# Optimization experiments

Hardware: AMD Instinct MI355X
Metric: run time of the kernel (lower is better)

Reference implementation:

```python
import jax, jax.numpy as jnp
import numpy as np

B, N, M = 16, 2048, 2048


def setup_inputs() -> dict:
    key = jax.random.key(0)
    k1, k2, k3 = jax.random.split(key, 3)
    pred_dsmat = jax.random.uniform(k1, (B, N, M), dtype=jnp.float32)
    # valid sizes: src_ns <= tgt_ns so a permutation GT exists for every valid row
    src_ns = jax.random.randint(k2, (B,), 1024, 1537, dtype=jnp.int32)
    tgt_ns = jax.random.randint(k3, (B,), 1537, 2049, dtype=jnp.int32)
    # gt_perm: identity permutation restricted to the valid region (one 1 per valid row)
    i = jnp.arange(N)[:, None]
    j = jnp.arange(M)[None, :]
    eye = (i == j).astype(jnp.float32)  # [N, M]
    row_mask = (jnp.arange(N)[None, :] < src_ns[:, None]).astype(jnp.float32)  # [B, N]
    gt_perm = eye[None, :, :] * row_mask[:, :, None]  # [B, N, M]
    return {"pred_dsmat": pred_dsmat, "gt_perm": gt_perm,
            "src_ns": src_ns, "tgt_ns": tgt_ns, "beta_value": 0.1}


def reference(pred_dsmat, gt_perm, src_ns, tgt_ns, beta_value):
    Bn, Nn, Mn = pred_dsmat.shape
    row_mask = jnp.arange(Nn)[None, :] < src_ns[:, None]   # [B, N] bool
    col_mask = jnp.arange(Mn)[None, :] < tgt_ns[:, None]   # [B, M] bool
    mask = row_mask[:, :, None] & col_mask[:, None, :]     # [B, N, M]

    pred = jnp.clip(pred_dsmat, 0.0, 1.0) * mask
    gt = gt_perm * mask

    gt_pred = pred * gt                      # gt-selected predicted values
    row_gt = gt_pred.sum(axis=2)             # [B, N] per-row GT value
    col_gt = gt_pred.sum(axis=1)             # [B, M] per-col GT value
    row_cnt = gt.sum(axis=2)                 # [B, N] #GT matches per row
    col_cnt = gt.sum(axis=1)                 # [B, M] #GT matches per col

    # attention masks: entries >= (gt value - beta), restricted to valid region
    att_src = ((pred >= row_gt[:, :, None] - beta_value) & mask) * row_cnt[:, :, None]
    att_tgt = ((pred >= col_gt[:, None, :] - beta_value) & mask) * col_cnt[:, None, :]

    src_neg = jnp.sum(((att_src - gt) * pred) ** 2, axis=2)  # [B, N]
    src_pos = jnp.sum(gt_pred ** 2, axis=2)                  # [B, N]
    tgt_neg = jnp.sum(((att_tgt - gt) * pred) ** 2, axis=1)  # [B, M]

    # sum of tgt_neg over the GT-matched column of each row == dot with column counts
    corr = jnp.einsum('bm,bm->b', tgt_neg, col_cnt)          # [B]

    denom = 1.0 + src_neg + corr[:, None]                    # [B, N]
    num = jnp.where(row_mask, src_pos, 1.0)
    den = jnp.where(row_mask, denom, 1.0)
    loss = -0.5 * jnp.sum(jnp.log(num / den) * row_mask)
    n_sum = src_ns.sum().astype(pred.dtype)
    return loss / n_sum
```

## Files before the change

### kernel.cpp

```cpp
#include <hip/hip_runtime.h>

#define B_ 16
#define N_ 2048
#define M_ 2048
#define ROWS 32
#define WROWS 8
#define KCAP 4

__device__ __forceinline__ float wave_sum(float v) {
#pragma unroll
    for (int off = 32; off >= 1; off >>= 1) v += __shfl_xor(v, off);
    return v;
}

extern "C" __global__ __launch_bounds__(256) void k_gt(
    const float* __restrict__ gt,
    const int* __restrict__ src_ns, const int* __restrict__ tgt_ns,
    int* __restrict__ nnz, int* __restrict__ ent_col,
    float* __restrict__ ent_val, int* flag)
{
    const int b = blockIdx.y;
    const int src = src_ns[b];
    const int band = blockIdx.x;
    if (band * ROWS >= src) return;
    const int tgt = tgt_ns[b];
    const int wave = threadIdx.x >> 6, lane = threadIdx.x & 63;
    const int base = b * (N_ * M_);
    const int jmax = (tgt + 255) >> 8;

    const int row0 = band * ROWS + wave * WROWS;
    for (int r = 0; r < WROWS; ++r) {
        const int n = row0 + r;
        if (n >= src) break;
        const int ri = b * N_ + n;
        const float4* grow = (const float4*)(gt + base + n * M_);
        for (int j = 0; j < jmax; ++j) {
            const int m4 = j * 64 + lane;
            const float4 g4 = grow[m4];
            if (g4.x != 0.f || g4.y != 0.f || g4.z != 0.f || g4.w != 0.f) {
                const int mb = m4 * 4;
#define GC(KK, MB) do { \
    const int c = mb + KK; \
    const float gv = g4.MB; \
    if (gv != 0.f && c < tgt) { \
        const int slot = atomicAdd(&nnz[ri], 1); \
        if (slot < KCAP) { ent_col[ri * KCAP + slot] = c; ent_val[ri * KCAP + slot] = gv; } \
        else *flag = 1; \
    } \
} while (0)
                GC(0, x); GC(1, y); GC(2, z); GC(3, w);
#undef GC
            }
        }
    }
}

extern "C" __global__ __launch_bounds__(256) void k_mid(
    const float* __restrict__ pred,
    const int* __restrict__ src_ns,
    const int* __restrict__ nnz, const int* __restrict__ ent_col,
    const float* __restrict__ ent_val, const int* flag,
    float* __restrict__ row_gt, float* __restrict__ row_cnt,
    float* __restrict__ col_gt, float* __restrict__ col_cnt)
{
    if (*flag) return;
    const int ri = blockIdx.x * 256 + threadIdx.x;
    const int b = ri >> 11, n = ri & (N_ - 1);
    if (n >= src_ns[b]) { row_gt[ri] = 0.f; row_cnt[ri] = 0.f; return; }
    const int nn0 = nnz[ri];
    const int nn = nn0 < KCAP ? nn0 : KCAP;
    float rg = 0.f, rc = 0.f;
    for (int s = 0; s < nn; ++s) {
        const int c = ent_col[ri * KCAP + s];
        const float gv = ent_val[ri * KCAP + s];
        float p = pred[b * (N_ * M_) + n * M_ + c];
        p = fminf(fmaxf(p, 0.f), 1.f);
        rg += gv * p; rc += gv;
        atomicAdd(&col_gt[b * M_ + c], gv * p);
        atomicAdd(&col_cnt[b * M_ + c], gv);
    }
    row_gt[ri] = rg; row_cnt[ri] = rc;
}

extern "C" __global__ __launch_bounds__(256) void k_p1d(
    const float* __restrict__ pred, const float* __restrict__ gt,
    const int* __restrict__ src_ns, const int* __restrict__ tgt_ns,
    const int* flag,
    float* __restrict__ row_gt, float* __restrict__ row_cnt,
    float* __restrict__ col_gt, float* __restrict__ col_cnt)
{
    if (*flag == 0) return;
    const int b = blockIdx.y;
    const int src = src_ns[b];
    const int band = blockIdx.x;
    if (band * ROWS >= src) return;
    const int tgt = tgt_ns[b];
    const int wave = threadIdx.x >> 6, lane = threadIdx.x & 63;
    const int base = b * (N_ * M_);

    float4 acg[8], accn[8];
#pragma unroll
    for (int j = 0; j < 8; ++j) { acg[j] = make_float4(0,0,0,0); accn[j] = make_float4(0,0,0,0); }

    const int row0 = band * ROWS + wave * WROWS;
    for (int r = 0; r < WROWS; ++r) {
        const int n = row0 + r;
        if (n >= src) break;
        const float4* prow = (const float4*)(pred + base + n * M_);
        const float4* grow = (const float4*)(gt + base + n * M_);
        float rg = 0.f, rc = 0.f;
#pragma unroll
        for (int j = 0; j < 8; ++j) {
            const int m4 = j * 64 + lane;
            const float4 p4 = prow[m4];
            const float4 g4 = grow[m4];
            const int mb = m4 * 4;
#define P1C(KK, MB) do { \
    const bool ok = (mb + KK) < tgt; \
    float p = fminf(fmaxf(p4.MB, 0.f), 1.f); p = ok ? p : 0.f; \
    const float g = ok ? g4.MB : 0.f; \
    const float gp = p * g; \
    rg += gp; rc += g; \
    acg[j].MB += gp; accn[j].MB += g; \
} while (0)
            P1C(0, x); P1C(1, y); P1C(2, z); P1C(3, w);
#undef P1C
        }
        rg = wave_sum(rg); rc = wave_sum(rc);
        if (lane == 0) { row_gt[b * N_ + n] = rg; row_cnt[b * N_ + n] = rc; }
    }

    __shared__ float4 s_cg[M_ / 4];
    __shared__ float4 s_cc[M_ / 4];
    for (int i = threadIdx.x; i < M_ / 4; i += 256) {
        s_cg[i] = make_float4(0,0,0,0);
        s_cc[i] = make_float4(0,0,0,0);
    }
    __syncthreads();
    for (int w = 0; w < 4; ++w) {
        if (wave == w) {
#pragma unroll
            for (int j = 0; j < 8; ++j) {
                const int i = j * 64 + lane;
                float4 v = s_cg[i];
                v.x += acg[j].x; v.y += acg[j].y; v.z += acg[j].z; v.w += acg[j].w;
                s_cg[i] = v;
                float4 u = s_cc[i];
                u.x += accn[j].x; u.y += accn[j].y; u.z += accn[j].z; u.w += accn[j].w;
                s_cc[i] = u;
            }
        }
        __syncthreads();
    }
    const float* fcg = (const float*)s_cg;
    const float* fcc = (const float*)s_cc;
    for (int i = threadIdx.x; i < M_; i += 256) {
        atomicAdd(&col_gt[b * M_ + i], fcg[i]);
        atomicAdd(&col_cnt[b * M_ + i], fcc[i]);
    }
}

extern "C" __global__ __launch_bounds__(256) void k_pred(
    const float* __restrict__ pred, const float* __restrict__ gt,
    const int* __restrict__ src_ns, const int* __restrict__ tgt_ns,
    const float* __restrict__ beta_p,
    const float* __restrict__ row_gt, const float* __restrict__ row_cnt,
    const float* __restrict__ col_gt, const float* __restrict__ col_cnt,
    const int* __restrict__ nnz, const int* __restrict__ ent_col,
    const float* __restrict__ ent_val, const int* flag,
    float* __restrict__ src_neg, float* __restrict__ src_pos,
    float* __restrict__ tgt_neg)
{
    const int b = blockIdx.y;
    const int src = src_ns[b];
    const int band = blockIdx.x;
    if (band * ROWS >= src) return;
    const int tgt = tgt_ns[b];
    const float beta = beta_p[0];
    const int wave = threadIdx.x >> 6, lane = threadIdx.x & 63;
    const int base = b * (N_ * M_);
    const bool dense = (*flag != 0);
    const int jmax = (tgt + 255) >> 8;

    float4 cgb[8], cc[8], tn[8];
    const float4* cg4 = (const float4*)(col_gt + b * M_);
    const float4* cc4 = (const float4*)(col_cnt + b * M_);
#pragma unroll
    for (int j = 0; j < 8; ++j) {
        float4 v = cg4[j * 64 + lane];
        v.x -= beta; v.y -= beta; v.z -= beta; v.w -= beta;
        cgb[j] = v;
        cc[j] = cc4[j * 64 + lane];
        tn[j] = make_float4(0,0,0,0);
    }

    const int row0 = band * ROWS + wave * WROWS;
    if (!dense) {
        for (int r = 0; r < WROWS; ++r) {
            const int n = row0 + r;
            if (n >= src) break;
            const int ri = b * N_ + n;
            const float rc = row_cnt[ri];
            const float rth = row_gt[ri] - beta;
            const float4* prow = (const float4*)(pred + base + n * M_);
            float sneg = 0.f, spos = 0.f;
#pragma unroll
            for (int j = 0; j < 8; ++j) {
                if (j < jmax) {
                    const int m4 = j * 64 + lane;
                    const float4 p4 = prow[m4];
                    const int mb = m4 * 4;
#define P2S(KK, MB) do { \
    const bool ok = (mb + KK) < tgt; \
    float p = fminf(fmaxf(p4.MB, 0.f), 1.f); p = ok ? p : 0.f; \
    const float as = (p >= rth) ? rc : 0.f; \
    const float ds = as * p; \
    sneg += ds * ds; \
    const float at = (p >= cgb[j].MB) ? cc[j].MB : 0.f; \
    const float d = at * p; \
    tn[j].MB += d * d; \
} while (0)
                    P2S(0, x); P2S(1, y); P2S(2, z); P2S(3, w);
#undef P2S
                }
            }
            sneg = wave_sum(sneg);
            if (lane == 0) {
                const int nn0 = nnz[ri];
                const int nn = nn0 < KCAP ? nn0 : KCAP;
                for (int s = 0; s < nn; ++s) {
                    const int c = ent_col[ri * KCAP + s];
                    const float gv = ent_val[ri * KCAP + s];
                    float pv = pred[base + n * M_ + c];
                    pv = fminf(fmaxf(pv, 0.f), 1.f);
                    const float as = (pv >= rth) ? rc : 0.f;
                    const float d0 = as * pv;
                    const float d1 = (as - gv) * pv;
                    sneg += d1 * d1 - d0 * d0;
                    const float gp = gv * pv;
                    spos += gp * gp;
                    const float at = (pv >= col_gt[b * M_ + c] - beta) ? col_cnt[b * M_ + c] : 0.f;
                    const float t0 = at * pv;
                    const float t1 = (at - gv) * pv;
                    atomicAdd(&tgt_neg[b * M_ + c], t1 * t1 - t0 * t0);
                }
                src_neg[ri] = sneg; src_pos[ri] = spos;
            }
        }
    } else {
        for (int r = 0; r < WROWS; ++r) {
            const int n = row0 + r;
            if (n >= src) break;
            const int ri = b * N_ + n;
            const float rc = row_cnt[ri];
            const float rth = row_gt[ri] - beta;
            const float4* prow = (const float4*)(pred + base + n * M_);
            const float4* grow = (const float4*)(gt + base + n * M_);
            float sneg = 0.f, spos = 0.f;
#pragma unroll
            for (int j = 0; j < 8; ++j) {
                const int m4 = j * 64 + lane;
                const float4 p4 = prow[m4];
                const float4 g4 = grow[m4];
                const int mb = m4 * 4;
#define P2D(KK, MB) do { \
    const bool ok = (mb + KK) < tgt; \
    float p = fminf(fmaxf(p4.MB, 0.f), 1.f); p = ok ? p : 0.f; \
    const float gv = ok ? g4.MB : 0.f; \
    const float as = (p >= rth) ? rc : 0.f; \
    const float ds = (as - gv) * p; \
    sneg += ds * ds; \
    const float gp = gv * p; spos += gp * gp; \
    const float at = (p >= cgb[j].MB) ? cc[j].MB : 0.f; \
    const float dt = (at - gv) * p; \
    tn[j].MB += dt * dt; \
} while (0)
                P2D(0, x); P2D(1, y); P2D(2, z); P2D(3, w);
#undef P2D
            }
            sneg = wave_sum(sneg); spos = wave_sum(spos);
            if (lane == 0) { src_neg[ri] = sneg; src_pos[ri] = spos; }
        }
    }

    __shared__ float4 s_tn[M_ / 4];
    for (int i = threadIdx.x; i < M_ / 4; i += 256) s_tn[i] = make_float4(0,0,0,0);
    __syncthreads();
    for (int w = 0; w < 4; ++w) {
        if (wave == w) {
#pragma unroll
            for (int j = 0; j < 8; ++j) {
                const int i = j * 64 + lane;
                float4 v = s_tn[i];
                v.x += tn[j].x; v.y += tn[j].y; v.z += tn[j].z; v.w += tn[j].w;
                s_tn[i] = v;
            }
        }
        __syncthreads();
    }
    const float* ftn = (const float*)s_tn;
    for (int i = threadIdx.x; i < M_; i += 256)
        atomicAdd(&tgt_neg[b * M_ + i], ftn[i]);
}

extern "C" __global__ __launch_bounds__(256) void k_final(
    const float* __restrict__ src_neg, const float* __restrict__ src_pos,
    const float* __restrict__ tgt_neg, const float* __restrict__ col_cnt,
    const int* __restrict__ src_ns, float* __restrict__ out)
{
    const int b = blockIdx.x;
    const int wave = threadIdx.x >> 6, lane = threadIdx.x & 63;
    __shared__ float sredc[4];
    __shared__ float sredl[4];

    float c = 0.f;
    for (int i = threadIdx.x; i < M_; i += 256)
        c += tgt_neg[b * M_ + i] * col_cnt[b * M_ + i];
    c = wave_sum(c);
    if (lane == 0) sredc[wave] = c;
    __syncthreads();
    const float corr = sredc[0] + sredc[1] + sredc[2] + sredc[3];

    const int src = src_ns[b];
    float ls = 0.f;
    for (int n = threadIdx.x; n < src; n += 256) {
        const float sp = src_pos[b * N_ + n];
        const float sn = src_neg[b * N_ + n];
        ls += logf(sp) - logf(1.f + sn + corr);
    }
    ls = wave_sum(ls);
    if (lane == 0) sredl[wave] = ls;
    __syncthreads();
    if (threadIdx.x == 0) {
        const float total = sredl[0] + sredl[1] + sredl[2] + sredl[3];
        float nsum = 0.f;
        for (int i = 0; i < B_; ++i) nsum += (float)src_ns[i];
        atomicAdd(out, -0.5f * total / nsum);
    }
}

extern "C" void kernel_launch(void* const* d_in, const int* in_sizes, int n_in,
                              void* d_out, int out_size, void* d_ws, size_t ws_size,
                              hipStream_t stream)
{
    const float* pred   = (const float*)d_in[0];
    const float* gtp    = (const float*)d_in[1];
    const int*   src_ns = (const int*)d_in[2];
    const int*   tgt_ns = (const int*)d_in[3];
    const float* beta   = (const float*)d_in[4];
    float* out = (float*)d_out;
    float* ws  = (float*)d_ws;

    float* col_gt  = ws;
    float* col_cnt = col_gt  + B_ * M_;
    float* tgt_neg = col_cnt + B_ * M_;
    int*   nnz     = (int*)(tgt_neg + B_ * M_);
    int*   flag    = nnz + B_ * N_;
    float* row_gt  = (float*)(flag + 1);
    float* row_cnt = row_gt  + B_ * N_;
    float* src_neg = row_cnt + B_ * N_;
    float* src_pos = src_neg + B_ * N_;
    int*   ent_col = (int*)(src_pos + B_ * N_);
    float* ent_val = (float*)(ent_col + B_ * N_ * KCAP);

    const size_t zero_bytes = (size_t)(3 * B_ * M_ + B_ * N_ + 1) * sizeof(float);
    hipMemsetAsync(d_ws, 0, zero_bytes, stream);
    hipMemsetAsync(d_out, 0, sizeof(float), stream);

    dim3 grid(N_ / ROWS, B_);
    k_gt<<<grid, 256, 0, stream>>>(gtp, src_ns, tgt_ns, nnz, ent_col, ent_val, flag);
    k_mid<<<(B_ * N_) / 256, 256, 0, stream>>>(pred, src_ns, nnz, ent_col, ent_val, flag,
                                               row_gt, row_cnt, col_gt, col_cnt);
    k_p1d<<<grid, 256, 0, stream>>>(pred, gtp, src_ns, tgt_ns, flag,
                                    row_gt, row_cnt, col_gt, col_cnt);
    k_pred<<<grid, 256, 0, stream>>>(pred, gtp, src_ns, tgt_ns, beta,
                                     row_gt, row_cnt, col_gt, col_cnt,
                                     nnz, ent_col, ent_val, flag,
                                     src_neg, src_pos, tgt_neg);
    k_final<<<B_, 256, 0, stream>>>(src_neg, src_pos, tgt_neg, col_cnt, src_ns, out);
}
```

Before: 581.2 us.

## Split gt scan and pred pass into column chunks with smaller row bands

Result: faster. 518.0 us (-10.9%).

```diff
diff --git a/kernel.cpp b/kernel.cpp
--- a/kernel.cpp
+++ b/kernel.cpp
@@ -3,8 +3,13 @@
 #define B_ 16
 #define N_ 2048
 #define M_ 2048
-#define ROWS 32
-#define WROWS 8
+#define RROWS 16
+#define WROWS 4
+#define CHUNK 1024
+#define NCHUNK (M_ / CHUNK)
+#define JCH (CHUNK / 256)
+#define DROWS 32
+#define DWROWS 8
 #define KCAP 4
 
 __device__ __forceinline__ float wave_sum(float v) {
@@ -22,23 +27,26 @@
     const int b = blockIdx.y;
     const int src = src_ns[b];
     const int band = blockIdx.x;
-    if (band * ROWS >= src) return;
+    if (band * RROWS >= src) return;
     const int tgt = tgt_ns[b];
+    const int c0 = blockIdx.z * CHUNK;
+    const int lim = tgt - c0;
+    if (lim <= 0) return;
+    const int jmaxL = lim >= CHUNK ? JCH : ((lim + 255) >> 8);
     const int wave = threadIdx.x >> 6, lane = threadIdx.x & 63;
-    const int base = b * (N_ * M_);
-    const int jmax = (tgt + 255) >> 8;
-
-    const int row0 = band * ROWS + wave * WROWS;
+    const int bc = b * (N_ * M_) + c0;
+
+    const int row0 = band * RROWS + wave * WROWS;
     for (int r = 0; r < WROWS; ++r) {
         const int n = row0 + r;
         if (n >= src) break;
         const int ri = b * N_ + n;
-        const float4* grow = (const float4*)(gt + base + n * M_);
-        for (int j = 0; j < jmax; ++j) {
+        const float4* grow = (const float4*)(gt + bc + n * M_);
+        for (int j = 0; j < jmaxL; ++j) {
             const int m4 = j * 64 + lane;
             const float4 g4 = grow[m4];
             if (g4.x != 0.f || g4.y != 0.f || g4.z != 0.f || g4.w != 0.f) {
-                const int mb = m4 * 4;
+                const int mb = c0 + m4 * 4;
 #define GC(KK, MB) do { \
     const int c = mb + KK; \
     const float gv = g4.MB; \
@@ -93,7 +101,7 @@
     const int b = blockIdx.y;
     const int src = src_ns[b];
     const int band = blockIdx.x;
-    if (band * ROWS >= src) return;
+    if (band * DROWS >= src) return;
     const int tgt = tgt_ns[b];
     const int wave = threadIdx.x >> 6, lane = threadIdx.x & 63;
     const int base = b * (N_ * M_);
@@ -102,8 +110,8 @@
 #pragma unroll
     for (int j = 0; j < 8; ++j) { acg[j] = make_float4(0,0,0,0); accn[j] = make_float4(0,0,0,0); }
 
-    const int row0 = band * ROWS + wave * WROWS;
-    for (int r = 0; r < WROWS; ++r) {
+    const int row0 = band * DROWS + wave * DWROWS;
+    for (int r = 0; r < DWROWS; ++r) {
         const int n = row0 + r;
         if (n >= src) break;
         const float4* prow = (const float4*)(pred + base + n * M_);
@@ -174,19 +182,24 @@
     const int b = blockIdx.y;
     const int src = src_ns[b];
     const int band = blockIdx.x;
-    if (band * ROWS >= src) return;
+    if (band * RROWS >= src) return;
     const int tgt = tgt_ns[b];
+    const int c0 = blockIdx.z * CHUNK;
+    const bool chunk0 = (c0 == 0);
+    const int lim = tgt - c0;
+    if (lim <= 0 && !chunk0) return;
+    const int jmaxL = lim >= CHUNK ? JCH : (lim > 0 ? ((lim + 255) >> 8) : 0);
     const float beta = beta_p[0];
     const int wave = threadIdx.x >> 6, lane = threadIdx.x & 63;
-    const int base = b * (N_ * M_);
+    const int bfull = b * (N_ * M_);
+    const int bc = bfull + c0;
     const bool dense = (*flag != 0);
-    const int jmax = (tgt + 255) >> 8;
-
-    float4 cgb[8], cc[8], tn[8];
-    const float4* cg4 = (const float4*)(col_gt + b * M_);
-    const float4* cc4 = (const float4*)(col_cnt + b * M_);
-#pragma unroll
-    for (int j = 0; j < 8; ++j) {
+
+    float4 cgb[JCH], cc[JCH], tn[JCH];
+    const float4* cg4 = (const float4*)(col_gt + b * M_ + c0);
+    const float4* cc4 = (const float4*)(col_cnt + b * M_ + c0);
+#pragma unroll
+    for (int j = 0; j < JCH; ++j) {
         float4 v = cg4[j * 64 + lane];
         v.x -= beta; v.y -= beta; v.z -= beta; v.w -= beta;
         cgb[j] = v;
@@ -194,7 +207,7 @@
         tn[j] = make_float4(0,0,0,0);
     }
 
-    const int row0 = band * ROWS + wave * WROWS;
+    const int row0 = band * RROWS + wave * WROWS;
     if (!dense) {
         for (int r = 0; r < WROWS; ++r) {
             const int n = row0 + r;
@@ -202,14 +215,14 @@
             const int ri = b * N_ + n;
             const float rc = row_cnt[ri];
             const float rth = row_gt[ri] - beta;
-            const float4* prow = (const float4*)(pred + base + n * M_);
-            float sneg = 0.f, spos = 0.f;
-#pragma unroll
-            for (int j = 0; j < 8; ++j) {
-                if (j < jmax) {
+            const float4* prow = (const float4*)(pred + bc + n * M_);
+            float sneg = 0.f;
+#pragma unroll
+            for (int j = 0; j < JCH; ++j) {
+                if (j < jmaxL) {
                     const int m4 = j * 64 + lane;
                     const float4 p4 = prow[m4];
-                    const int mb = m4 * 4;
+                    const int mb = c0 + m4 * 4;
 #define P2S(KK, MB) do { \
     const bool ok = (mb + KK) < tgt; \
     float p = fminf(fmaxf(p4.MB, 0.f), 1.f); p = ok ? p : 0.f; \
@@ -226,25 +239,29 @@
             }
             sneg = wave_sum(sneg);
             if (lane == 0) {
-                const int nn0 = nnz[ri];
-                const int nn = nn0 < KCAP ? nn0 : KCAP;
-                for (int s = 0; s < nn; ++s) {
-                    const int c = ent_col[ri * KCAP + s];
-                    const float gv = ent_val[ri * KCAP + s];
-                    float pv = pred[base + n * M_ + c];
-                    pv = fminf(fmaxf(pv, 0.f), 1.f);
-                    const float as = (pv >= rth) ? rc : 0.f;
-                    const float d0 = as * pv;
-                    const float d1 = (as - gv) * pv;
-                    sneg += d1 * d1 - d0 * d0;
-                    const float gp = gv * pv;
-                    spos += gp * gp;
-                    const float at = (pv >= col_gt[b * M_ + c] - beta) ? col_cnt[b * M_ + c] : 0.f;
-                    const float t0 = at * pv;
-                    const float t1 = (at - gv) * pv;
-                    atomicAdd(&tgt_neg[b * M_ + c], t1 * t1 - t0 * t0);
+                if (chunk0) {
+                    float spos = 0.f;
+                    const int nn0 = nnz[ri];
+                    const int nn = nn0 < KCAP ? nn0 : KCAP;
+                    for (int s = 0; s < nn; ++s) {
+                        const int c = ent_col[ri * KCAP + s];
+                        const float gv = ent_val[ri * KCAP + s];
+                        float pv = pred[bfull + n * M_ + c];
+                        pv = fminf(fmaxf(pv, 0.f), 1.f);
+                        const float as = (pv >= rth) ? rc : 0.f;
+                        const float d0 = as * pv;
+                        const float d1 = (as - gv) * pv;
+                        sneg += d1 * d1 - d0 * d0;
+                        const float gp = gv * pv;
+                        spos += gp * gp;
+                        const float at = (pv >= col_gt[b * M_ + c] - beta) ? col_cnt[b * M_ + c] : 0.f;
+                        const float t0 = at * pv;
+                        const float t1 = (at - gv) * pv;
+                        atomicAdd(&tgt_neg[b * M_ + c], t1 * t1 - t0 * t0);
+                    }
+                    atomicAdd(&src_pos[ri], spos);
                 }
-                src_neg[ri] = sneg; src_pos[ri] = spos;
+                atomicAdd(&src_neg[ri], sneg);
             }
         }
     } else {
@@ -254,15 +271,16 @@
             const int ri = b * N_ + n;
             const float rc = row_cnt[ri];
             const float rth = row_gt[ri] - beta;
-            const float4* prow = (const float4*)(pred + base + n * M_);
-            const float4* grow = (const float4*)(gt + base + n * M_);
+            const float4* prow = (const float4*)(pred + bc + n * M_);
+            const float4* grow = (const float4*)(gt + bc + n * M_);
             float sneg = 0.f, spos = 0.f;
 #pragma unroll
-            for (int j = 0; j < 8; ++j) {
-                const int m4 = j * 64 + lane;
-                const float4 p4 = prow[m4];
-                const float4 g4 = grow[m4];
-                const int mb = m4 * 4;
+            for (int j = 0; j < JCH; ++j) {
+                if (j < jmaxL) {
+                    const int m4 = j * 64 + lane;
+                    const float4 p4 = prow[m4];
+                    const float4 g4 = grow[m4];
+                    const int mb = c0 + m4 * 4;
 #define P2D(KK, MB) do { \
     const bool ok = (mb + KK) < tgt; \
     float p = fminf(fmaxf(p4.MB, 0.f), 1.f); p = ok ? p : 0.f; \
@@ -275,21 +293,25 @@
     const float dt = (at - gv) * p; \
     tn[j].MB += dt * dt; \
 } while (0)
-                P2D(0, x); P2D(1, y); P2D(2, z); P2D(3, w);
+                    P2D(0, x); P2D(1, y); P2D(2, z); P2D(3, w);
 #undef P2D
+                }
             }
             sneg = wave_sum(sneg); spos = wave_sum(spos);
-            if (lane == 0) { src_neg[ri] = sneg; src_pos[ri] = spos; }
-        }
-    }
-
-    __shared__ float4 s_tn[M_ / 4];
-    for (int i = threadIdx.x; i < M_ / 4; i += 256) s_tn[i] = make_float4(0,0,0,0);
+            if (lane == 0) {
+                atomicAdd(&src_neg[ri], sneg);
+                atomicAdd(&src_pos[ri], spos);
+            }
+        }
+    }
+
+    __shared__ float4 s_tn[CHUNK / 4];
+    for (int i = threadIdx.x; i < CHUNK / 4; i += 256) s_tn[i] = make_float4(0,0,0,0);
     __syncthreads();
     for (int w = 0; w < 4; ++w) {
         if (wave == w) {
 #pragma unroll
-            for (int j = 0; j < 8; ++j) {
+            for (int j = 0; j < JCH; ++j) {
                 const int i = j * 64 + lane;
                 float4 v = s_tn[i];
                 v.x += tn[j].x; v.y += tn[j].y; v.z += tn[j].z; v.w += tn[j].w;
@@ -299,8 +321,8 @@
         __syncthreads();
     }
     const float* ftn = (const float*)s_tn;
-    for (int i = threadIdx.x; i < M_; i += 256)
-        atomicAdd(&tgt_neg[b * M_ + i], ftn[i]);
+    for (int i = threadIdx.x; i < CHUNK; i += 256)
+        atomicAdd(&tgt_neg[b * M_ + c0 + i], ftn[i]);
 }
 
 extern "C" __global__ __launch_bounds__(256) void k_final(
@@ -354,28 +376,28 @@
     float* col_gt  = ws;
     float* col_cnt = col_gt  + B_ * M_;
     float* tgt_neg = col_cnt + B_ * M_;
-    int*   nnz     = (int*)(tgt_neg + B_ * M_);
+    float* src_neg = tgt_neg + B_ * M_;
+    float* src_pos = src_neg + B_ * N_;
+    int*   nnz     = (int*)(src_pos + B_ * N_);
     int*   flag    = nnz + B_ * N_;
     float* row_gt  = (float*)(flag + 1);
-    float* row_cnt = row_gt  + B_ * N_;
-    float* src_neg = row_cnt + B_ * N_;
-    float* src_pos = src_neg + B_ * N_;
-    int*   ent_col = (int*)(src_pos + B_ * N_);
+    float* row_cnt = row_gt + B_ * N_;
+    int*   ent_col = (int*)(row_cnt + B_ * N_);
     float* ent_val = (float*)(ent_col + B_ * N_ * KCAP);
 
-    const size_t zero_bytes = (size_t)(3 * B_ * M_ + B_ * N_ + 1) * sizeof(float);
+    const size_t zero_bytes = (size_t)(3 * B_ * M_ + 3 * B_ * N_ + 1) * sizeof(float);
     hipMemsetAsync(d_ws, 0, zero_bytes, stream);
     hipMemsetAsync(d_out, 0, sizeof(float), stream);
 
-    dim3 grid(N_ / ROWS, B_);
-    k_gt<<<grid, 256, 0, stream>>>(gtp, src_ns, tgt_ns, nnz, ent_col, ent_val, flag);
+    dim3 gsplit(N_ / RROWS, B_, NCHUNK);
+    k_gt<<<gsplit, 256, 0, stream>>>(gtp, src_ns, tgt_ns, nnz, ent_col, ent_val, flag);
     k_mid<<<(B_ * N_) / 256, 256, 0, stream>>>(pred, src_ns, nnz, ent_col, ent_val, flag,
                                                row_gt, row_cnt, col_gt, col_cnt);
-    k_p1d<<<grid, 256, 0, stream>>>(pred, gtp, src_ns, tgt_ns, flag,
-                                    row_gt, row_cnt, col_gt, col_cnt);
-    k_pred<<<grid, 256, 0, stream>>>(pred, gtp, src_ns, tgt_ns, beta,
-                                     row_gt, row_cnt, col_gt, col_cnt,
-                                     nnz, ent_col, ent_val, flag,
-                                     src_neg, src_pos, tgt_neg);
+    k_p1d<<<dim3(N_ / DROWS, B_), 256, 0, stream>>>(pred, gtp, src_ns, tgt_ns, flag,
+                                                    row_gt, row_cnt, col_gt, col_cnt);
+    k_pred<<<gsplit, 256, 0, stream>>>(pred, gtp, src_ns, tgt_ns, beta,
+                                       row_gt, row_cnt, col_gt, col_cnt,
+                                       nnz, ent_col, ent_val, flag,
+                                       src_neg, src_pos, tgt_neg);
     k_final<<<B_, 256, 0, stream>>>(src_neg, src_pos, tgt_neg, col_cnt, src_ns, out);
 }
```
